# Kernel optimization log

Hardware: AMD Instinct MI355X
Metric: run time of the kernel (lower is better)

Reference implementation:

```python
import jax, jax.numpy as jnp
import numpy as np

INF = 1.0e12
V, EMB, H, H2 = 50000, 300, 512, 1024
EDGE, EEMB = 4, 32
B, TS, TQ = 16, 400, 33
MAX_OOV = 100
EXT = V + MAX_OOV
COV_HYPER = 1.0


def gru_cell(x, h, Wi, Wh, bi, bh):
    # torch GRU cell, gate order r,z,n
    gx = x @ Wi.T + bi
    gh = h @ Wh.T + bh
    hd = h.shape[-1]
    r = jax.nn.sigmoid(gx[:, :hd] + gh[:, :hd])
    z = jax.nn.sigmoid(gx[:, hd:2 * hd] + gh[:, hd:2 * hd])
    n = jnp.tanh(gx[:, 2 * hd:] + r * gh[:, 2 * hd:])
    return (1.0 - z) * n + z * h


def gru_scan(xs, h0, Wi, Wh, bi, bh, reverse=False):
    def step(h, x):
        hn = gru_cell(x, h, Wi, Wh, bi, bh)
        return hn, hn
    return jax.lax.scan(step, h0, xs, reverse=reverse)


def setup_inputs() -> dict:
    key = jax.random.key(0)
    ks = iter(jax.random.split(key, 64))
    def rp(*shape):
        return jax.random.normal(next(ks), shape, jnp.float32) * 0.05
    d = {}
    d['enc_emb'] = rp(V, EMB); d['ans_emb'] = rp(EDGE, EEMB); d['dec_emb'] = rp(V, EMB)
    in0 = EMB + EEMB
    d['eWi0'] = rp(2, 3 * H, in0); d['eWh0'] = rp(2, 3 * H, H); d['ebi0'] = rp(2, 3 * H); d['ebh0'] = rp(2, 3 * H)
    d['eWi1'] = rp(2, 3 * H, 2 * H); d['eWh1'] = rp(2, 3 * H, H); d['ebi1'] = rp(2, 3 * H); d['ebh1'] = rp(2, 3 * H)
    d['trans_W'] = rp(H2, H2); d['trans_b'] = rp(H2)
    d['upd_W'] = rp(H2, 2 * H2); d['gate_W'] = rp(H2, 2 * H2)
    din0 = EMB + H2
    d['dWi0'] = rp(3 * H2, din0); d['dWh0'] = rp(3 * H2, H2); d['dbi0'] = rp(3 * H2); d['dbh0'] = rp(3 * H2)
    d['dWi1'] = rp(3 * H2, H2); d['dWh1'] = rp(3 * H2, H2); d['dbi1'] = rp(3 * H2); d['dbh1'] = rp(3 * H2)
    d['dtrans_W'] = rp(H2, H2); d['dtrans_b'] = rp(H2)
    d['pW1'] = rp(H2, 2 * H2); d['pb1'] = rp(H2); d['pW2'] = rp(V, H2); d['pb2'] = rp(V)
    d['input_s'] = jax.random.randint(next(ks), (B, TS), 1, V)
    ext = jax.random.randint(next(ks), (B, TS), 0, EXT)
    d['ext_src_ids'] = ext.at[0, 0].set(EXT - 1)  # pin num_oov = MAX_OOV
    d['input_q'] = jax.random.randint(next(ks), (B, TQ), 1, V)
    d['input_a'] = jax.random.randint(next(ks), (B, TS), 0, EDGE)
    d['s_pos'] = jax.random.randint(next(ks), (B, TS), 0, TS)
    return d


def reference(enc_emb, ans_emb, dec_emb,
              eWi0, eWh0, ebi0, ebh0, eWi1, eWh1, ebi1, ebh1,
              trans_W, trans_b, upd_W, gate_W,
              dWi0, dWh0, dbi0, dbh0, dWi1, dWh1, dbi1, dbh1,
              dtrans_W, dtrans_b, pW1, pb1, pW2, pb2,
              input_s, ext_src_ids, input_q, input_a, s_pos):
    mask = jnp.sign(input_s)  # [B,TS] (all ones by construction)
    # ---------------- encoder ----------------
    emb = jnp.concatenate([enc_emb[input_s], ans_emb[input_a]], -1)  # [B,TS,EMB+EEMB]
    xs = emb.transpose(1, 0, 2)  # [TS,B,*]
    h0 = jnp.zeros((B, H), emb.dtype)
    h_list = []
    for (Wi, Wh, bi, bh) in ((eWi0, eWh0, ebi0, ebh0), (eWi1, eWh1, ebi1, ebh1)):
        hf, yf = gru_scan(xs, h0, Wi[0], Wh[0], bi[0], bh[0])
        hb, yb = gru_scan(xs, h0, Wi[1], Wh[1], bi[1], bh[1], reverse=True)
        xs = jnp.concatenate([yf, yb], -1)
        h_list.append(jnp.concatenate([hf, hb], -1))  # [B,H2]
    output = xs.transpose(1, 0, 2)  # [B,TS,H2]
    memories = output @ trans_W.T + trans_b
    # gated self-attention
    energies = jnp.einsum('btd,bsd->bts', output, memories)
    energies = jnp.where(mask[:, None, :] == 0, -INF, energies)
    scores = jax.nn.softmax(energies, -1)
    ctx = jnp.einsum('bts,bsd->btd', scores, output)
    inp = jnp.concatenate([output, ctx], -1)
    f_t = jnp.tanh(inp @ upd_W.T)
    g_t = jax.nn.sigmoid(inp @ gate_W.T)
    self_out = g_t * f_t + (1.0 - g_t) * output
    # answer-sentence attention (on memories, per original code)
    ans = jnp.where(input_a[..., None] == 0, 1.0, memories)
    e = memories * ans
    e = jnp.where(mask[..., None] == 0, -INF, e)
    e = jax.nn.softmax(e, axis=1)
    enc_out = self_out + e * memories
    # ---------------- decoder ----------------
    mem_d = enc_out @ dtrans_W.T + dtrans_b  # [B,TS,H2]
    emb_q = dec_emb[input_q[:, :-1]].transpose(1, 0, 2)  # [Tt,B,EMB]
    b_idx = jnp.arange(B)[:, None]

    def step(carry, emb_t):
        h0c, h1c, ctx_c, cov = carry
        rnn_in = jnp.concatenate([emb_t, ctx_c], -1)
        h0n = gru_cell(rnn_in, h0c, dWi0, dWh0, dbi0, dbh0)
        h1n = gru_cell(h0n, h1c, dWi1, dWh1, dbi1, dbh1)
        energy = jnp.einsum('bd,btd->bt', h1n, mem_d)
        sen_e = jnp.where(mask == 0, -INF, energy)
        cov_e = sen_e * (1.0 - cov)
        attn = jax.nn.softmax(cov_e, -1)
        new_ctx = jnp.einsum('bt,btd->bd', attn, mem_d)
        cov_loss = jnp.sum(jnp.minimum(attn, cov)) / B * COV_HYPER
        new_cov = cov + attn
        hid = jnp.tanh(jnp.concatenate([h1n, new_ctx], -1) @ pW1.T + pb1)
        logits = hid @ pW2.T + pb2
        ext = jnp.concatenate([logits, jnp.zeros((B, MAX_OOV), logits.dtype)], -1)
        out = jnp.full((B, EXT), -INF, logits.dtype).at[b_idx, ext_src_ids].max(cov_e)
        out = jnp.where(out == -INF, 0.0, out)
        lg = ext + out
        lg = jnp.where(lg == 0.0, -INF, lg)
        return (h0n, h1n, new_ctx, new_cov), (lg, cov_loss)

    init = (h_list[0], h_list[1], jnp.zeros((B, H2), emb.dtype), jnp.zeros((B, TS), emb.dtype))
    _, (lgs, covl) = jax.lax.scan(step, init, emb_q)
    return lgs.transpose(1, 0, 2), jnp.sum(covl) / lgs.shape[0]


if __name__ == '__main__':
    o = reference(**setup_inputs())
    print(o[0].shape, o[1])
```

## Files before the change

kernel.cpp:

```cpp
#include <hip/hip_runtime.h>
#include <stdint.h>

#define TSN 400
#define NB 16
#define HENC 512
#define HD2 1024
#define G3E 1536
#define G3D 3072
#define EMBD 300
#define AEMB 32
#define NV 50000
#define NEXT 50100
#define NVP 50176
#define NTT 32
#define NEG_INF (-1.0e12f)

typedef __attribute__((ext_vector_type(8))) short bf16x8;
typedef __attribute__((ext_vector_type(4))) float f32x4;

__device__ __forceinline__ ushort f2bf(float f) {
  unsigned u = __float_as_uint(f);
  unsigned r = (u + 0x7fffu + ((u >> 16) & 1u)) >> 16;
  return (ushort)r;
}
__device__ __forceinline__ float bf2f(ushort h) {
  return __uint_as_float((unsigned)h << 16);
}
__device__ __forceinline__ unsigned agat_ld(const unsigned* p) {
  return __hip_atomic_load(p, __ATOMIC_RELAXED, __HIP_MEMORY_SCOPE_AGENT);
}
__device__ __forceinline__ void agat_st(unsigned* p, unsigned v) {
  __hip_atomic_store(p, v, __ATOMIC_RELAXED, __HIP_MEMORY_SCOPE_AGENT);
}

__global__ __launch_bounds__(256) void k_embed_bf(
    const float* __restrict__ enc_emb, const float* __restrict__ ans_emb,
    const int* __restrict__ input_s, const int* __restrict__ input_a,
    ushort* __restrict__ X0)
{
  long i = (long)blockIdx.x*256 + threadIdx.x;
  if (i >= (long)TSN*NB*384) return;
  int c = (int)(i % 384);
  long r = i / 384;
  int b = (int)(r % NB);
  int t = (int)(r / NB);
  float v = 0.f;
  if (c < EMBD) v = enc_emb[(long)input_s[b*TSN + t]*EMBD + c];
  else if (c < 332) v = ans_emb[(long)input_a[b*TSN + t]*AEMB + (c - EMBD)];
  X0[i] = f2bf(v);
}

__global__ __launch_bounds__(256) void k_embq_bf(
    const float* __restrict__ dec_emb, const int* __restrict__ input_q,
    ushort* __restrict__ EQ)
{
  long i = (long)blockIdx.x*256 + threadIdx.x;
  if (i >= (long)NTT*NB*320) return;
  int c = (int)(i % 320);
  long r = i / 320;
  int b = (int)(r % NB);
  int s = (int)(r / NB);
  EQ[i] = (c < EMBD) ? f2bf(dec_emb[(long)input_q[b*33 + s]*EMBD + c]) : (ushort)0;
}

__global__ __launch_bounds__(256) void k_castw(
    const float* __restrict__ src, ushort* __restrict__ dst,
    int Nsrc, long total, int Ksrc, int Kdst, int ldsrc, int coloff)
{
  long i = (long)blockIdx.x*256 + threadIdx.x;
  if (i >= total) return;
  int k = (int)(i % Kdst);
  long n = i / Kdst;
  float v = (n < Nsrc && k < Ksrc) ? src[n*ldsrc + coloff + k] : 0.f;
  dst[i] = f2bf(v);
}

__global__ __launch_bounds__(256) void k_cast(
    const float* __restrict__ s, ushort* __restrict__ d, long n)
{
  long i = (long)blockIdx.x*256 + threadIdx.x;
  if (i >= n) return;
  d[i] = f2bf(s[i]);
}

__global__ __launch_bounds__(256) void k_catcopy(
    const unsigned* __restrict__ src, unsigned* __restrict__ dst)
{
  long i = (long)blockIdx.x*256 + threadIdx.x;
  if (i >= 6400l*512) return;
  long r = i >> 9;
  int c = (int)(i & 511);
  dst[(r << 10) + c] = src[i];
}

__global__ __launch_bounds__(256) void k_transpose_hh(
    const ushort* __restrict__ in, ushort* __restrict__ out)
{
  __shared__ ushort tb[32][33];
  int b = blockIdx.z;
  int r0 = blockIdx.x*32, c0 = blockIdx.y*32;
  int tx = threadIdx.x & 31, ty = threadIdx.x >> 5;
  #pragma unroll
  for (int i = 0; i < 32; i += 8) {
    int r = r0 + ty + i, c = c0 + tx;
    tb[ty+i][tx] = (r < TSN) ? in[((long)b*TSN + r)*1024 + c] : (ushort)0;
  }
  __syncthreads();
  #pragma unroll
  for (int i = 0; i < 32; i += 8) {
    int c = c0 + ty + i, r = r0 + tx;
    out[((long)b*1024 + c)*448 + r] = tb[tx][ty+i];
  }
}

__global__ __launch_bounds__(256) void k_mfma_nt(
    const ushort* __restrict__ Ab, const ushort* __restrict__ Wb,
    const float* __restrict__ bias, float* __restrict__ Cb, ushort* __restrict__ C2b,
    int M, int N, int K, int lda, int ldw, int ldc,
    long sA, long sW, long sC, long sBias, int accum, int act)
{
  __shared__ ushort As[64][72];
  __shared__ ushort Ws[64][72];
  const ushort* A = Ab + (long)blockIdx.z * sA;
  const ushort* W = Wb + (long)blockIdx.z * sW;
  float* C = Cb ? Cb + (long)blockIdx.z * sC : nullptr;
  const float* bi = bias ? bias + (long)blockIdx.z * sBias : nullptr;
  const int m0 = blockIdx.x*64, n0 = blockIdx.y*64;
  const int tid = threadIdx.x;
  const int wave = tid >> 6, lane = tid & 63;
  const int wm = wave >> 1, wn = wave & 1;
  const int lr = lane & 15, kg = lane >> 4;
  f32x4 acc[2][2] = {};
  for (int k0 = 0; k0 < K; k0 += 64) {
    __syncthreads();
    #pragma unroll
    for (int it = 0; it < 2; ++it) {
      int sidx = tid + it*256;
      int r = sidx >> 3, c = (sidx & 7)*8;
      bf16x8 av = {};
      bf16x8 wv = {};
      if (m0 + r < M) av = *(const bf16x8*)&A[(long)(m0+r)*lda + k0 + c];
      if (n0 + r < N) wv = *(const bf16x8*)&W[(long)(n0+r)*ldw + k0 + c];
      *(bf16x8*)&As[r][c] = av;
      *(bf16x8*)&Ws[r][c] = wv;
    }
    __syncthreads();
    #pragma unroll
    for (int kk = 0; kk < 2; ++kk) {
      bf16x8 af[2], bf[2];
      #pragma unroll
      for (int mt = 0; mt < 2; ++mt)
        af[mt] = *(const bf16x8*)&As[wm*32 + mt*16 + lr][kk*32 + kg*8];
      #pragma unroll
      for (int nt = 0; nt < 2; ++nt)
        bf[nt] = *(const bf16x8*)&Ws[wn*32 + nt*16 + lr][kk*32 + kg*8];
      #pragma unroll
      for (int mt = 0; mt < 2; ++mt)
        #pragma unroll
        for (int nt = 0; nt < 2; ++nt)
          acc[mt][nt] = __builtin_amdgcn_mfma_f32_16x16x32_bf16(af[mt], bf[nt], acc[mt][nt], 0, 0, 0);
    }
  }
  #pragma unroll
  for (int mt = 0; mt < 2; ++mt) {
    #pragma unroll
    for (int r = 0; r < 4; ++r) {
      int m = m0 + wm*32 + mt*16 + kg*4 + r;
      if (m >= M) continue;
      #pragma unroll
      for (int nt = 0; nt < 2; ++nt) {
        int n = n0 + wn*32 + nt*16 + lr;
        if (n >= N) continue;
        float v = acc[mt][nt][r];
        if (accum && C) v += C[(long)m*ldc + n];
        if (bi)    v += bi[n];
        if (act == 1) v = tanhf(v);
        else if (act == 2) v = 1.f/(1.f + expf(-v));
        if (C) C[(long)m*ldc + n] = v;
        if (C2b) C2b[(long)blockIdx.z*sC + (long)m*ldc + n] = f2bf(v);
      }
    }
  }
}

__global__ __launch_bounds__(256, 1) void k_scan_mfma(
    const ushort* __restrict__ GXf, const ushort* __restrict__ GXb,
    const ushort* __restrict__ Whb,
    const float* __restrict__ bh,
    ushort* __restrict__ Ybf, int bmajor,
    float* __restrict__ hfin,
    ushort* __restrict__ hpp,
    int* __restrict__ slots)
{
  const int bid = blockIdx.x;
  const int tid = threadIdx.x;
  const int wg = bid*4 + (tid >> 6);
  const int lane = tid & 63;
  const int lr = lane & 15, kg = lane >> 4;
  const int dir = wg >> 5, jt = wg & 31;
  const int j = jt*16 + lr;
  __shared__ ushort hsm[16][520];
  const ushort* Wp0 = Whb + ((long)(dir*G3E + j)        << 9) + kg*8;
  const ushort* Wp1 = Whb + ((long)(dir*G3E + 512 + j)  << 9) + kg*8;
  const ushort* Wp2 = Whb + ((long)(dir*G3E + 1024 + j) << 9) + kg*8;
  bf16x8 W0[16], W1[16], W2[16];
  #pragma unroll
  for (int i = 0; i < 16; ++i) {
    W0[i] = *(const bf16x8*)(Wp0 + i*32);
    W1[i] = *(const bf16x8*)(Wp1 + i*32);
    W2[i] = *(const bf16x8*)(Wp2 + i*32);
  }
  const float bh0 = bh[dir*G3E + j];
  const float bh1 = bh[dir*G3E + 512 + j];
  const float bh2 = bh[dir*G3E + 1024 + j];
  const ushort* GX = dir ? GXb : GXf;
  unsigned* hppu = (unsigned*)hpp;
  int* myslot = slots + dir*256 + (bid & 7)*32;
  int* dslots = slots + dir*256;
  float hreg[4] = {0.f, 0.f, 0.f, 0.f};
  float g0[4], g1[4], g2[4];
  {
    const int t0 = dir ? (TSN - 1) : 0;
    const ushort* gxp = GX + (long)t0*NB*G3E + j;
    #pragma unroll
    for (int r = 0; r < 4; ++r) {
      const ushort* g = gxp + (long)(kg*4 + r)*G3E;
      g0[r] = bf2f(g[0]); g1[r] = bf2f(g[512]); g2[r] = bf2f(g[1024]);
    }
  }
  for (int s = 0; s < TSN; ++s) {
    const int cur = s & 1;
    {
      const unsigned* hin = hppu + (cur*2 + dir)*4096;
      unsigned vdw[16];
      #pragma unroll
      for (int i = 0; i < 16; ++i) vdw[i] = agat_ld(hin + i*256 + tid);
      #pragma unroll
      for (int i = 0; i < 16; ++i) {
        int idx = i*256 + tid;
        int b = idx >> 8, jd = idx & 255;
        *(unsigned*)&hsm[b][jd*2] = vdw[i];
      }
    }
    __syncthreads();
    f32x4 a0 = {}, a1 = {}, a2 = {};
    #pragma unroll
    for (int i = 0; i < 16; ++i) {
      bf16x8 hf = *(const bf16x8*)&hsm[lr][kg*8 + i*32];
      a0 = __builtin_amdgcn_mfma_f32_16x16x32_bf16(hf, W0[i], a0, 0, 0, 0);
      a1 = __builtin_amdgcn_mfma_f32_16x16x32_bf16(hf, W1[i], a1, 0, 0, 0);
      a2 = __builtin_amdgcn_mfma_f32_16x16x32_bf16(hf, W2[i], a2, 0, 0, 0);
    }
    const int t = dir ? (TSN - 1 - s) : s;
    const int obase = ((cur^1)*2 + dir)*16*512;
    float hsave[4];
    #pragma unroll
    for (int r = 0; r < 4; ++r) {
      int b = kg*4 + r;
      float rr = 1.f/(1.f + expf(-(g0[r] + a0[r] + bh0)));
      float zz = 1.f/(1.f + expf(-(g1[r] + a1[r] + bh1)));
      float nn = tanhf(g2[r] + rr*(a2[r] + bh2));
      float hn = (1.f - zz)*nn + zz*hreg[r];
      hreg[r] = hn;
      hsave[r] = hn;
      unsigned hv = f2bf(hn);
      unsigned pv = (unsigned)__shfl_xor((int)hv, 1);
      if ((lr & 1) == 0)
        agat_st(hppu + ((obase + b*512 + j) >> 1), hv | (pv << 16));
    }
    if (s + 1 < TSN) {
      asm volatile("s_waitcnt vmcnt(0)" ::: "memory");
      __syncthreads();
      if (tid == 0)
        agat_st((unsigned*)myslot, (unsigned)(s + 1));
      {
        const int tn = dir ? (TSN - 2 - s) : (s + 1);
        const ushort* gxp = GX + (long)tn*NB*G3E + j;
        #pragma unroll
        for (int r = 0; r < 4; ++r) {
          const ushort* g = gxp + (long)(kg*4 + r)*G3E;
          g0[r] = bf2f(g[0]); g1[r] = bf2f(g[512]); g2[r] = bf2f(g[1024]);
        }
      }
      #pragma unroll
      for (int r = 0; r < 4; ++r) {
        int b = kg*4 + r;
        long yi = bmajor ? ((long)b*TSN + t)*1024 + dir*512 + j
                         : ((long)t*NB + b)*1024 + dir*512 + j;
        Ybf[yi] = f2bf(hsave[r]);
      }
      if (tid < 8) {
        while ((int)agat_ld((const unsigned*)(dslots + tid*32)) < s + 1)
          __builtin_amdgcn_s_sleep(1);
      }
      __syncthreads();
    } else {
      #pragma unroll
      for (int r = 0; r < 4; ++r) {
        int b = kg*4 + r;
        long yi = bmajor ? ((long)b*TSN + t)*1024 + dir*512 + j
                         : ((long)t*NB + b)*1024 + dir*512 + j;
        Ybf[yi] = f2bf(hsave[r]);
        hfin[b*1024 + dir*512 + j] = hsave[r];
      }
    }
  }
}

__global__ __launch_bounds__(256) void k_softmax_bf(
    const float* __restrict__ E, ushort* __restrict__ S)
{
  long row = blockIdx.x;
  const float* x = E + row*TSN;
  ushort* o = S + row*448;
  int tid = threadIdx.x;
  float v0 = (tid < TSN) ? x[tid] : -INFINITY;
  float v1 = (tid + 256 < TSN) ? x[tid + 256] : -INFINITY;
  __shared__ float red[256];
  red[tid] = fmaxf(v0, v1); __syncthreads();
  for (int oo = 128; oo; oo >>= 1) { if (tid < oo) red[tid] = fmaxf(red[tid], red[tid+oo]); __syncthreads(); }
  float m = red[0]; __syncthreads();
  float e0 = (tid < TSN) ? expf(v0 - m) : 0.f;
  float e1 = (tid + 256 < TSN) ? expf(v1 - m) : 0.f;
  red[tid] = e0 + e1; __syncthreads();
  for (int oo = 128; oo; oo >>= 1) { if (tid < oo) red[tid] += red[tid+oo]; __syncthreads(); }
  float inv = 1.f/red[0];
  if (tid < 192) o[tid + 256] = (tid + 256 < TSN) ? f2bf(e1*inv) : (ushort)0;
  o[tid] = f2bf(e0*inv);
}

__global__ __launch_bounds__(256) void k_ansatt2(
    const ushort* __restrict__ memsb, const ushort* __restrict__ ftgt,
    const ushort* __restrict__ outpb,
    const int* __restrict__ input_a, ushort* __restrict__ encb)
{
  int b = blockIdx.x >> 2;
  int d = (blockIdx.x & 3)*256 + threadIdx.x;
  __shared__ int ia[TSN];
  for (int i = threadIdx.x; i < TSN; i += 256) ia[i] = input_a[b*TSN + i];
  __syncthreads();
  float m = -INFINITY;
  #pragma unroll 4
  for (int t = 0; t < TSN; ++t) {
    float v = bf2f(memsb[((long)b*TSN + t)*1024 + d]);
    float e = ia[t] ? v*v : v;
    m = fmaxf(m, e);
  }
  float ssum = 0.f;
  #pragma unroll 4
  for (int t = 0; t < TSN; ++t) {
    float v = bf2f(memsb[((long)b*TSN + t)*1024 + d]);
    float e = ia[t] ? v*v : v;
    ssum += expf(e - m);
  }
  float inv = 1.f/ssum;
  #pragma unroll 4
  for (int t = 0; t < TSN; ++t) {
    long idx = ((long)b*TSN + t)*1024 + d;
    long idx2 = ((long)b*TSN + t)*2048 + d;
    float v = bf2f(memsb[idx]);
    float e = ia[t] ? v*v : v;
    float fraw = bf2f(ftgt[idx2]);
    float graw = bf2f(ftgt[idx2 + 1024]);
    float gg = 1.f/(1.f + expf(-graw));
    float selfo = gg*tanhf(fraw) + (1.f - gg)*bf2f(outpb[idx]);
    encb[idx] = f2bf(selfo + expf(e - m)*inv*v);
  }
}

__global__ __launch_bounds__(128) void k_gru_dec(
    const ushort* __restrict__ A1, const ushort* __restrict__ W1,
    const ushort* __restrict__ A2, const ushort* __restrict__ W2,
    const float* __restrict__ gxadd, const float* __restrict__ bi,
    const float* __restrict__ bh,
    const float* __restrict__ hprev, float* __restrict__ hout,
    ushort* __restrict__ houtb, ushort* __restrict__ catb)
{
  const int wv = threadIdx.x >> 6;
  const int lane = threadIdx.x & 63;
  const int lr = lane & 15, kg = lane >> 4;
  const int j = blockIdx.x*16 + lr;
  const int kb = wv*512;
  __shared__ float psum[6][16][16];
  const ushort* w1p0 = W1 + ((long)(j)        << 10) + kb + kg*8;
  const ushort* w1p1 = W1 + ((long)(1024 + j) << 10) + kb + kg*8;
  const ushort* w1p2 = W1 + ((long)(2048 + j) << 10) + kb + kg*8;
  const ushort* w2p0 = W2 + ((long)(j)        << 10) + kb + kg*8;
  const ushort* w2p1 = W2 + ((long)(1024 + j) << 10) + kb + kg*8;
  const ushort* w2p2 = W2 + ((long)(2048 + j) << 10) + kb + kg*8;
  const ushort* a1p = A1 + lr*1024 + kb + kg*8;
  const ushort* a2p = A2 + lr*1024 + kb + kg*8;
  f32x4 x0 = {}, x1 = {}, x2 = {}, h0 = {}, h1 = {}, h2 = {};
  #pragma unroll 4
  for (int k0 = 0; k0 < 512; k0 += 32) {
    bf16x8 a1v = *(const bf16x8*)(a1p + k0);
    bf16x8 a2v = *(const bf16x8*)(a2p + k0);
    x0 = __builtin_amdgcn_mfma_f32_16x16x32_bf16(a1v, *(const bf16x8*)(w1p0 + k0), x0, 0, 0, 0);
    x1 = __builtin_amdgcn_mfma_f32_16x16x32_bf16(a1v, *(const bf16x8*)(w1p1 + k0), x1, 0, 0, 0);
    x2 = __builtin_amdgcn_mfma_f32_16x16x32_bf16(a1v, *(const bf16x8*)(w1p2 + k0), x2, 0, 0, 0);
    h0 = __builtin_amdgcn_mfma_f32_16x16x32_bf16(a2v, *(const bf16x8*)(w2p0 + k0), h0, 0, 0, 0);
    h1 = __builtin_amdgcn_mfma_f32_16x16x32_bf16(a2v, *(const bf16x8*)(w2p1 + k0), h1, 0, 0, 0);
    h2 = __builtin_amdgcn_mfma_f32_16x16x32_bf16(a2v, *(const bf16x8*)(w2p2 + k0), h2, 0, 0, 0);
  }
  if (wv == 1) {
    #pragma unroll
    for (int r = 0; r < 4; ++r) {
      int b = kg*4 + r;
      psum[0][b][lr] = x0[r]; psum[1][b][lr] = x1[r]; psum[2][b][lr] = x2[r];
      psum[3][b][lr] = h0[r]; psum[4][b][lr] = h1[r]; psum[5][b][lr] = h2[r];
    }
  }
  __syncthreads();
  if (wv == 0) {
    float bi0 = bi ? bi[j] : 0.f, bi1 = bi ? bi[1024 + j] : 0.f, bi2 = bi ? bi[2048 + j] : 0.f;
    float bh0 = bh[j], bh1 = bh[1024 + j], bh2 = bh[2048 + j];
    #pragma unroll
    for (int r = 0; r < 4; ++r) {
      int b = kg*4 + r;
      float gxa0 = gxadd ? gxadd[(long)b*G3D + j]        : 0.f;
      float gxa1 = gxadd ? gxadd[(long)b*G3D + 1024 + j] : 0.f;
      float gxa2 = gxadd ? gxadd[(long)b*G3D + 2048 + j] : 0.f;
      float gx0 = x0[r] + psum[0][b][lr] + gxa0 + bi0;
      float gx1 = x1[r] + psum[1][b][lr] + gxa1 + bi1;
      float gx2 = x2[r] + psum[2][b][lr] + gxa2 + bi2;
      float gh0 = h0[r] + psum[3][b][lr] + bh0;
      float gh1 = h1[r] + psum[4][b][lr] + bh1;
      float gh2 = h2[r] + psum[5][b][lr] + bh2;
      float rr = 1.f/(1.f + expf(-(gx0 + gh0)));
      float zz = 1.f/(1.f + expf(-(gx1 + gh1)));
      float nn = tanhf(gx2 + rr*gh2);
      float hp = hprev[b*1024 + j];
      float hn = (1.f - zz)*nn + zz*hp;
      hout[b*1024 + j] = hn;
      houtb[b*1024 + j] = f2bf(hn);
      if (catb) catb[(long)b*2048 + j] = f2bf(hn);
    }
  }
}

__global__ __launch_bounds__(256) void k_dec_attn3(
    const ushort* __restrict__ h1b, const ushort* __restrict__ memdb,
    float* __restrict__ cov, float* __restrict__ coveS, float* __restrict__ covacc,
    float* __restrict__ scb,
    ushort* __restrict__ ctxn, ushort* __restrict__ catb,
    int* __restrict__ slots, int epoch)
{
  const int bid = blockIdx.x, tid = threadIdx.x;
  const int b = bid >> 2, q = bid & 3;
  const int wv = tid >> 6, lane = tid & 63;
  __shared__ float at[TSN];
  __shared__ float red[256];
  __shared__ float psD[4][64][4];
  float hr[16];
  {
    bf16x8 hv0 = *(const bf16x8*)&h1b[b*1024 + lane*16];
    bf16x8 hv1 = *(const bf16x8*)&h1b[b*1024 + lane*16 + 8];
    #pragma unroll
    for (int e = 0; e < 8; ++e) { hr[e] = bf2f((ushort)hv0[e]); hr[8+e] = bf2f((ushort)hv1[e]); }
// ... 89 lines not shown
  const int lr = lane & 15, kg = lane >> 4;
  const int n = blockIdx.x*16 + lr;
  const int kb = wv*1024;
  __shared__ float ps[16][16];
  f32x4 acc = {};
  const ushort* ap = catb + lr*2048 + kb + kg*8;
  const ushort* wp = W + ((long)n << 11) + kb + kg*8;
  #pragma unroll 8
  for (int k0 = 0; k0 < 1024; k0 += 32)
    acc = __builtin_amdgcn_mfma_f32_16x16x32_bf16(*(const bf16x8*)(ap + k0), *(const bf16x8*)(wp + k0), acc, 0, 0, 0);
  if (wv == 1) {
    #pragma unroll
    for (int r = 0; r < 4; ++r) ps[kg*4 + r][lr] = acc[r];
  }
  __syncthreads();
  if (wv == 0) {
    float bv = pb1[n];
    #pragma unroll
    for (int r = 0; r < 4; ++r) {
      int b = kg*4 + r;
      hidb[b*1024 + n] = f2bf(tanhf(acc[r] + ps[b][lr] + bv));
    }
  }
}

__global__ __launch_bounds__(256) void k_logits_all(
    const ushort* __restrict__ hidAll,
    const ushort* __restrict__ pW2b,
    const float* __restrict__ pb2,
    float* __restrict__ outp)
{
  const int wave = threadIdx.x >> 6, lane = threadIdx.x & 63;
  const int lr = lane & 15, kg = lane >> 4;
  const int n0 = blockIdx.x*256 + wave*64;
  const int m0 = blockIdx.y*128;
  f32x4 acc[8][4] = {};
  for (int k0 = 0; k0 < 1024; k0 += 32) {
    bf16x8 bfr[4];
    #pragma unroll
    for (int nt = 0; nt < 4; ++nt)
      bfr[nt] = *(const bf16x8*)&pW2b[(long)(n0 + nt*16 + lr)*1024 + k0 + kg*8];
    #pragma unroll
    for (int mt = 0; mt < 8; ++mt) {
      bf16x8 af = *(const bf16x8*)&hidAll[(long)(m0 + mt*16 + lr)*1024 + k0 + kg*8];
      #pragma unroll
      for (int nt = 0; nt < 4; ++nt)
        acc[mt][nt] = __builtin_amdgcn_mfma_f32_16x16x32_bf16(af, bfr[nt], acc[mt][nt], 0, 0, 0);
    }
  }
  #pragma unroll
  for (int nt = 0; nt < 4; ++nt) {
    int v = n0 + nt*16 + lr;
    if (v >= NEXT) continue;
    float pb = (v < NV) ? pb2[v] : 0.f;
    #pragma unroll
    for (int mt = 0; mt < 8; ++mt) {
      #pragma unroll
      for (int r = 0; r < 4; ++r) {
        int m = m0 + mt*16 + kg*4 + r;
        int s = m >> 4, b = m & 15;
        float e = (v < NV) ? (acc[mt][nt][r] + pb) : 0.f;
        if (e == 0.f) e = NEG_INF;
        outp[((long)b*NTT + s)*NEXT + v] = e;
      }
    }
  }
}

__device__ __forceinline__ float dec_f(unsigned e) {
  return (e & 0x80000000u) ? __uint_as_float(e ^ 0x80000000u) : __uint_as_float(~e);
}
__global__ __launch_bounds__(512) void k_compose_all(
    const int* __restrict__ ids, const float* __restrict__ coveAll,
    unsigned* __restrict__ ubuf, float* __restrict__ outp)
{
  int b = blockIdx.x, tid = threadIdx.x;
  int v = 0;
  if (tid < TSN) v = ids[b*TSN + tid];
  unsigned* up = ubuf + (long)b*NEXT;
  for (int s = 0; s < NTT; ++s) {
    if (tid < TSN) {
      float ce = coveAll[((long)s*NB + b)*TSN + tid];
      unsigned bb = __float_as_uint(ce);
      unsigned enc = (bb & 0x80000000u) ? ~bb : (bb | 0x80000000u);
      atomicMax(&up[v], enc);
    }
    __syncthreads();
    if (tid < TSN) {
      unsigned u = __hip_atomic_load(&up[v], __ATOMIC_RELAXED, __HIP_MEMORY_SCOPE_AGENT);
      float o = dec_f(u);
      long oi = ((long)b*NTT + s)*NEXT + v;
      float e = outp[oi];
      if (e == NEG_INF) e = 0.f;
      float lg = e + o;
      if (lg == 0.f) lg = NEG_INF;
      outp[oi] = lg;
    }
    __syncthreads();
    if (tid < TSN)
      __hip_atomic_store(&up[v], 0u, __ATOMIC_RELAXED, __HIP_MEMORY_SCOPE_AGENT);
    __syncthreads();
  }
}

__global__ void k_covout(const float* __restrict__ covacc, float* __restrict__ outp)
{
  outp[(long)NB*NTT*NEXT] = covacc[0] * (1.0f/(NB*NTT));
}

extern "C" void kernel_launch(void* const* d_in, const int* in_sizes, int n_in,
                              void* d_out, int out_size, void* d_ws, size_t ws_size,
                              hipStream_t stream) {
  (void)in_sizes; (void)n_in; (void)out_size; (void)ws_size;
  const float* enc_emb = (const float*)d_in[0];
  const float* ans_emb = (const float*)d_in[1];
  const float* dec_emb = (const float*)d_in[2];
  const float* eWi0 = (const float*)d_in[3];
  const float* eWh0 = (const float*)d_in[4];
  const float* ebi0 = (const float*)d_in[5];
  const float* ebh0 = (const float*)d_in[6];
  const float* eWi1 = (const float*)d_in[7];
  const float* eWh1 = (const float*)d_in[8];
  const float* ebi1 = (const float*)d_in[9];
  const float* ebh1 = (const float*)d_in[10];
  const float* trans_W = (const float*)d_in[11];
  const float* trans_b = (const float*)d_in[12];
  const float* upd_W = (const float*)d_in[13];
  const float* gate_W = (const float*)d_in[14];
  const float* dWi0 = (const float*)d_in[15];
  const float* dWh0 = (const float*)d_in[16];
  const float* dbi0 = (const float*)d_in[17];
  const float* dbh0 = (const float*)d_in[18];
  const float* dWi1 = (const float*)d_in[19];
  const float* dWh1 = (const float*)d_in[20];
  const float* dbi1 = (const float*)d_in[21];
  const float* dbh1 = (const float*)d_in[22];
  const float* dtrans_W = (const float*)d_in[23];
  const float* dtrans_b = (const float*)d_in[24];
  const float* pW1 = (const float*)d_in[25];
  const float* pb1 = (const float*)d_in[26];
  const float* pW2 = (const float*)d_in[27];
  const float* pb2 = (const float*)d_in[28];
  const int* input_s = (const int*)d_in[29];
  const int* ext_ids = (const int*)d_in[30];
  const int* input_q = (const int*)d_in[31];
  const int* input_a = (const int*)d_in[32];
  float* out = (float*)d_out;

  float* ws = (float*)d_ws;
  size_t off = 0;
  auto alloc = [&](size_t n) { float* p = ws + off; off += (n + 15) & ~(size_t)15; return p; };
  auto alloch = [&](size_t nh) { return (ushort*)alloc((nh + 1) / 2); };

  ushort* hpp  = alloch(2ull*2*NB*HENC);
  int*   bar   = (int*)alloc(4096);
  float* covacc= alloc(4);
  float* cov   = alloc(NB*TSN);
  float* scb   = alloc(NB*TSN);
  unsigned* ubuf = (unsigned*)alloc((size_t)NB*NEXT);
  float* hfin0 = alloc(NB*HD2);
  float* hfin1 = alloc(NB*HD2);
  float* dh0   = alloc(2ull*NB*HD2);
  float* dh1   = alloc(2ull*NB*HD2);
  ushort* h0b  = alloch(2ull*NB*HD2);
  ushort* h1b  = alloch(2ull*NB*HD2);
  ushort* ctxbf= alloch(2ull*NB*HD2);
  ushort* catbf= alloch((size_t)NB*2048);
  ushort* hidAll = alloch((size_t)NTT*NB*HD2);
  float* coveAll = alloc((size_t)NTT*NB*TSN);

  ushort* eWi0c   = alloch(2ull*G3E*384);
  ushort* eWi1c   = alloch(2ull*G3E*1024);
  ushort* Whb0    = alloch(2ull*G3E*HENC);
  ushort* Whb1    = alloch(2ull*G3E*HENC);
  ushort* transWb = alloch(1024ull*1024);
  ushort* fgWb    = alloch(2048ull*2048);
  ushort* dtransWb= alloch(1024ull*1024);
  ushort* dWi0e   = alloch(3072ull*320);
  ushort* dWi0c   = alloch(3072ull*1024);
  ushort* dWh0b   = alloch(3072ull*1024);
  ushort* dWi1b   = alloch(3072ull*1024);
  ushort* dWh1b   = alloch(3072ull*1024);
  ushort* pW1b    = alloch(1024ull*2048);

  size_t regionStart = off;
  float*  GXr  = alloc(2ull*6400*G3E);
  ushort* GXbf = (ushort*)GXr;
  ushort* X0c  = alloch(6400ull*384);
  ushort* Y0bf = alloch(6400ull*1024);
  alloc(6400ull*HD2);
  ushort* ftgt_bf = (ushort*)(ws + regionStart);
  ushort* pW2b    = (ushort*)(ws + regionStart);
  ushort* outpTb  = (ushort*)(ws + regionStart + 26000000);

  ushort* outpbf = alloch(6400ull*HD2);
  ushort* memsbf = alloch(6400ull*HD2);
  ushort* catE   = alloch(6400ull*2048);
  float*  energ  = alloc((size_t)NB*TSN*TSN);
  ushort* scoresb= alloch((size_t)NB*TSN*448);
  ushort* memd_bf= alloch(6400ull*HD2);
  ushort* encbf  = alloch(6400ull*HD2);
  ushort* embqb  = alloch(512ull*320);
  float*  embGX  = alloc(512ull*G3D);

  k_embed_bf<<<9600, 256, 0, stream>>>(enc_emb, ans_emb, input_s, input_a, X0c);
  k_castw<<<4608, 256, 0, stream>>>(eWi0, eWi0c, 3072, 3072ull*384, 332, 384, 332, 0);
  k_castw<<<12288, 256, 0, stream>>>(eWi1, eWi1c, 3072, 3072ull*1024, 1024, 1024, 1024, 0);
  k_castw<<<6144, 256, 0, stream>>>(eWh0, Whb0, 3072, 3072ull*512, 512, 512, 512, 0);
  k_castw<<<6144, 256, 0, stream>>>(eWh1, Whb1, 3072, 3072ull*512, 512, 512, 512, 0);
  k_castw<<<4096, 256, 0, stream>>>(trans_W, transWb, 1024, 1024ull*1024, 1024, 1024, 1024, 0);
  k_castw<<<8192, 256, 0, stream>>>(upd_W,  fgWb,              1024, 1024ull*2048, 2048, 2048, 2048, 0);
  k_castw<<<8192, 256, 0, stream>>>(gate_W, fgWb + 1024ull*2048, 1024, 1024ull*2048, 2048, 2048, 2048, 0);
  k_castw<<<4096, 256, 0, stream>>>(dtrans_W, dtransWb, 1024, 1024ull*1024, 1024, 1024, 1024, 0);
  k_castw<<<3840, 256, 0, stream>>>(dWi0, dWi0e, 3072, 3072ull*320, 300, 320, 1324, 0);
  k_castw<<<12288, 256, 0, stream>>>(dWi0, dWi0c, 3072, 3072ull*1024, 1024, 1024, 1324, 300);
  k_castw<<<12288, 256, 0, stream>>>(dWh0, dWh0b, 3072, 3072ull*1024, 1024, 1024, 1024, 0);
  k_castw<<<12288, 256, 0, stream>>>(dWi1, dWi1b, 3072, 3072ull*1024, 1024, 1024, 1024, 0);
  k_castw<<<12288, 256, 0, stream>>>(dWh1, dWh1b, 3072, 3072ull*1024, 1024, 1024, 1024, 0);
  k_castw<<<8192, 256, 0, stream>>>(pW1, pW1b, 1024, 1024ull*2048, 2048, 2048, 2048, 0);

  hipMemsetAsync(bar, 0, 16384, stream);

  k_mfma_nt<<<dim3(100,24,2), 256, 0, stream>>>(X0c, eWi0c, ebi0, nullptr, GXbf,
      6400, G3E, 384, 384, 384, G3E, 0, (long)G3E*384, 6400ull*G3E, G3E, 0, 0);
  hipMemsetAsync(hpp, 0, 2ull*2*NB*HENC*2, stream);
  k_scan_mfma<<<16, 256, 0, stream>>>(GXbf, GXbf + 6400ull*G3E, Whb0, ebh0,
      Y0bf, 0, hfin0, hpp, bar);
  k_mfma_nt<<<dim3(100,24,2), 256, 0, stream>>>(Y0bf, eWi1c, ebi1, nullptr, GXbf,
      6400, G3E, 1024, 1024, 1024, G3E, 0, (long)G3E*1024, 6400ull*G3E, G3E, 0, 0);
  hipMemsetAsync(hpp, 0, 2ull*2*NB*HENC*2, stream);
  k_scan_mfma<<<16, 256, 0, stream>>>(GXbf, GXbf + 6400ull*G3E, Whb1, ebh1,
      outpbf, 1, hfin1, hpp, bar + 512);

  k_mfma_nt<<<dim3(100,16,1), 256, 0, stream>>>(outpbf, transWb, trans_b, nullptr, memsbf,
      6400, HD2, 1024, 1024, 1024, HD2, 0, 0, 0, 0, 0, 0);
  k_mfma_nt<<<dim3(7,7,16), 256, 0, stream>>>(outpbf, memsbf, nullptr, energ, nullptr,
      TSN, TSN, 1024, 1024, 1024, TSN, (long)TSN*1024, (long)TSN*1024, (long)TSN*TSN, 0, 0, 0);
  k_softmax_bf<<<NB*TSN, 256, 0, stream>>>(energ, scoresb);
  k_transpose_hh<<<dim3(14,32,16), 256, 0, stream>>>(outpbf, outpTb);
  k_mfma_nt<<<dim3(7,16,16), 256, 0, stream>>>(scoresb, outpTb, nullptr, nullptr, catE + 1024,
      TSN, HD2, 448, 448, 448, 2048, (long)TSN*448, (long)HD2*448, (long)TSN*2048, 0, 0, 0);
  k_catcopy<<<12800, 256, 0, stream>>>((const unsigned*)outpbf, (unsigned*)catE);
  k_mfma_nt<<<dim3(100,32,1), 256, 0, stream>>>(catE, fgWb, nullptr, nullptr, ftgt_bf,
      6400, 2048, 2048, 2048, 2048, 2048, 0, 0, 0, 0, 0, 0);
  k_ansatt2<<<64, 256, 0, stream>>>(memsbf, ftgt_bf, outpbf, input_a, encbf);
  k_castw<<<200704, 256, 0, stream>>>(pW2, pW2b, NV, (long)NVP*1024, 1024, 1024, 1024, 0);
  k_mfma_nt<<<dim3(100,16,1), 256, 0, stream>>>(encbf, dtransWb, dtrans_b, nullptr, memd_bf,
      6400, HD2, 1024, 1024, 1024, HD2, 0, 0, 0, 0, 0, 0);

  k_embq_bf<<<640, 256, 0, stream>>>(dec_emb, input_q, embqb);
  k_mfma_nt<<<dim3(8,48,1), 256, 0, stream>>>(embqb, dWi0e, dbi0, embGX, nullptr,
      NTT*NB, G3D, 320, 320, 320, G3D, 0, 0, 0, 0, 0, 0);

  hipMemsetAsync(cov, 0, (size_t)NB*TSN*4, stream);
  hipMemsetAsync(covacc, 0, 4, stream);
  hipMemsetAsync(ubuf, 0, (size_t)NB*NEXT*4, stream);
  hipMemsetAsync(ctxbf, 0, (size_t)NB*HD2*2, stream);
  hipMemcpyAsync(dh0, hfin0, (size_t)NB*HD2*4, hipMemcpyDeviceToDevice, stream);
  hipMemcpyAsync(dh1, hfin1, (size_t)NB*HD2*4, hipMemcpyDeviceToDevice, stream);
  k_cast<<<64, 256, 0, stream>>>(hfin0, h0b, 16384);
  k_cast<<<64, 256, 0, stream>>>(hfin1, h1b, 16384);

  for (int s = 0; s < NTT; ++s) {
    int cur = s & 1, nxt = cur ^ 1;
    float* h0c = dh0 + (size_t)cur*NB*HD2;  float* h0n = dh0 + (size_t)nxt*NB*HD2;
    float* h1c = dh1 + (size_t)cur*NB*HD2;  float* h1n = dh1 + (size_t)nxt*NB*HD2;
    ushort* h0bc = h0b + (size_t)cur*NB*HD2; ushort* h0bn = h0b + (size_t)nxt*NB*HD2;
    ushort* h1bc = h1b + (size_t)cur*NB*HD2; ushort* h1bn = h1b + (size_t)nxt*NB*HD2;
    ushort* ctxc = ctxbf + (size_t)cur*NB*HD2; ushort* ctxn = ctxbf + (size_t)nxt*NB*HD2;

    k_gru_dec<<<64, 128, 0, stream>>>(ctxc, dWi0c, h0bc, dWh0b,
        embGX + (size_t)s*NB*G3D, nullptr, dbh0, h0c, h0n, h0bn, nullptr);
    k_gru_dec<<<64, 128, 0, stream>>>(h0bn, dWi1b, h1bc, dWh1b,
        nullptr, dbi1, dbh1, h1c, h1n, h1bn, catbf);
    k_dec_attn3<<<64, 256, 0, stream>>>(h1bn, memd_bf,
        cov, coveAll + (size_t)s*NB*TSN, covacc, scb, ctxn, catbf,
        bar + 1024, s + 1);
    k_hid<<<64, 128, 0, stream>>>(catbf, pW1b, pb1, hidAll + (size_t)s*NB*HD2);
  }
  k_logits_all<<<dim3(196, 4), 256, 0, stream>>>(hidAll, pW2b, pb2, out);
  k_compose_all<<<NB, 512, 0, stream>>>(ext_ids, coveAll, ubuf, out);
  k_covout<<<1, 1, 0, stream>>>(covacc, out);
}
```

Measured before the change: 6.001 ms.

## Replace cross-block MFMA GRU scan with per-batch fp16 dot2 scan kernels

```diff
diff --git a/kernel.cpp b/kernel.cpp
--- a/kernel.cpp
+++ b/kernel.cpp
@@ -17,6 +17,7 @@
 
 typedef __attribute__((ext_vector_type(8))) short bf16x8;
 typedef __attribute__((ext_vector_type(4))) float f32x4;
+typedef _Float16 f16x2 __attribute__((ext_vector_type(2)));
 
 __device__ __forceinline__ ushort f2bf(float f) {
   unsigned u = __float_as_uint(f);
@@ -31,6 +32,9 @@
 }
 __device__ __forceinline__ void agat_st(unsigned* p, unsigned v) {
   __hip_atomic_store(p, v, __ATOMIC_RELAXED, __HIP_MEMORY_SCOPE_AGENT);
+}
+__device__ __forceinline__ f16x2 u2h(unsigned u) {
+  union { unsigned x; f16x2 h; } c; c.x = u; return c.h;
 }
 
 __global__ __launch_bounds__(256) void k_embed_bf(
@@ -73,6 +77,26 @@
   long n = i / Kdst;
   float v = (n < Nsrc && k < Ksrc) ? src[n*ldsrc + coloff + k] : 0.f;
   dst[i] = f2bf(v);
+}
+
+__global__ __launch_bounds__(256) void k_castw_scan(
+    const float* __restrict__ src, unsigned* __restrict__ dst)
+{
+  long i = (long)blockIdx.x*256 + threadIdx.x;
+  if (i >= 786432l) return;
+  int dir = (int)(i / 393216);
+  int rem = (int)(i % 393216);
+  int p = rem / 1536;
+  int q = rem % 1536;
+  int jp = q / 6;
+  int g2 = q % 6;
+  int g = g2 >> 1, je = g2 & 1;
+  int row = g*512 + 2*jp + je;
+  const float* s = src + (long)dir*1536*512 + (long)row*512 + 2*p;
+  union { _Float16 h[2]; unsigned u; } c;
+  c.h[0] = (_Float16)s[0];
+  c.h[1] = (_Float16)s[1];
+  dst[i] = c.u;
 }
 
 __global__ __launch_bounds__(256) void k_cast(
@@ -183,127 +207,73 @@
   }
 }
 
-__global__ __launch_bounds__(256, 1) void k_scan_mfma(
+__global__ __launch_bounds__(256, 1) void k_scan_seq(
     const ushort* __restrict__ GXf, const ushort* __restrict__ GXb,
-    const ushort* __restrict__ Whb,
+    const unsigned* __restrict__ Wv,
     const float* __restrict__ bh,
     ushort* __restrict__ Ybf, int bmajor,
-    float* __restrict__ hfin,
-    ushort* __restrict__ hpp,
-    int* __restrict__ slots)
+    float* __restrict__ hfin)
 {
   const int bid = blockIdx.x;
+  const int b = bid >> 1, dir = bid & 1;
   const int tid = threadIdx.x;
-  const int wg = bid*4 + (tid >> 6);
-  const int lane = tid & 63;
-  const int lr = lane & 15, kg = lane >> 4;
-  const int dir = wg >> 5, jt = wg & 31;
-  const int j = jt*16 + lr;
-  __shared__ ushort hsm[16][520];
-  const ushort* Wp0 = Whb + ((long)(dir*G3E + j)        << 9) + kg*8;
-  const ushort* Wp1 = Whb + ((long)(dir*G3E + 512 + j)  << 9) + kg*8;
-  const ushort* Wp2 = Whb + ((long)(dir*G3E + 1024 + j) << 9) + kg*8;
-  bf16x8 W0[16], W1[16], W2[16];
-  #pragma unroll
-  for (int i = 0; i < 16; ++i) {
-    W0[i] = *(const bf16x8*)(Wp0 + i*32);
-    W1[i] = *(const bf16x8*)(Wp1 + i*32);
-    W2[i] = *(const bf16x8*)(Wp2 + i*32);
-  }
-  const float bh0 = bh[dir*G3E + j];
-  const float bh1 = bh[dir*G3E + 512 + j];
-  const float bh2 = bh[dir*G3E + 1024 + j];
+  const int j0 = 2*tid;
+  __shared__ unsigned hbuf[2][256];
   const ushort* GX = dir ? GXb : GXf;
-  unsigned* hppu = (unsigned*)hpp;
-  int* myslot = slots + dir*256 + (bid & 7)*32;
-  int* dslots = slots + dir*256;
-  float hreg[4] = {0.f, 0.f, 0.f, 0.f};
-  float g0[4], g1[4], g2[4];
-  {
-    const int t0 = dir ? (TSN - 1) : 0;
-    const ushort* gxp = GX + (long)t0*NB*G3E + j;
-    #pragma unroll
-    for (int r = 0; r < 4; ++r) {
-      const ushort* g = gxp + (long)(kg*4 + r)*G3E;
-      g0[r] = bf2f(g[0]); g1[r] = bf2f(g[512]); g2[r] = bf2f(g[1024]);
-    }
-  }
+  const unsigned* wbase = Wv + (long)dir*393216 + tid*6;
+  const float br0 = bh[dir*G3E + j0],        br1 = bh[dir*G3E + j0 + 1];
+  const float bz0 = bh[dir*G3E + 512 + j0],  bz1 = bh[dir*G3E + 512 + j0 + 1];
+  const float bn0 = bh[dir*G3E + 1024 + j0], bn1 = bh[dir*G3E + 1024 + j0 + 1];
+  float h0 = 0.f, h1 = 0.f;
+  hbuf[0][tid] = 0u;
+  __syncthreads();
   for (int s = 0; s < TSN; ++s) {
     const int cur = s & 1;
+    const int t = dir ? (TSN - 1 - s) : s;
+    const unsigned* gxp = (const unsigned*)(GX + ((long)t*NB + b)*G3E);
+    unsigned gr = gxp[tid];
+    unsigned gz = gxp[256 + tid];
+    unsigned gn = gxp[512 + tid];
+    float a0 = 0.f, a1 = 0.f, a2 = 0.f, a3 = 0.f, a4 = 0.f, a5 = 0.f;
+    const unsigned* wp = wbase;
+    const unsigned* hl = hbuf[cur];
+    #pragma unroll 4
+    for (int p = 0; p < 256; ++p) {
+      f16x2 hh = u2h(hl[p]);
+      a0 = __builtin_amdgcn_fdot2(hh, u2h(wp[0]), a0, false);
+      a1 = __builtin_amdgcn_fdot2(hh, u2h(wp[1]), a1, false);
+      a2 = __builtin_amdgcn_fdot2(hh, u2h(wp[2]), a2, false);
+      a3 = __builtin_amdgcn_fdot2(hh, u2h(wp[3]), a3, false);
+      a4 = __builtin_amdgcn_fdot2(hh, u2h(wp[4]), a4, false);
+      a5 = __builtin_amdgcn_fdot2(hh, u2h(wp[5]), a5, false);
+      wp += 1536;
+    }
+    float gr0 = bf2f((ushort)(gr & 0xffffu)), gr1 = bf2f((ushort)(gr >> 16));
+    float gz0 = bf2f((ushort)(gz & 0xffffu)), gz1 = bf2f((ushort)(gz >> 16));
+    float gn0 = bf2f((ushort)(gn & 0xffffu)), gn1 = bf2f((ushort)(gn >> 16));
+    float r0 = 1.f/(1.f + expf(-(gr0 + a0 + br0)));
+    float r1 = 1.f/(1.f + expf(-(gr1 + a1 + br1)));
+    float z0 = 1.f/(1.f + expf(-(gz0 + a2 + bz0)));
+    float z1 = 1.f/(1.f + expf(-(gz1 + a3 + bz1)));
+    float n0 = tanhf(gn0 + r0*(a4 + bn0));
+    float n1 = tanhf(gn1 + r1*(a5 + bn1));
+    float hn0 = (1.f - z0)*n0 + z0*h0;
+    float hn1 = (1.f - z1)*n1 + z1*h1;
+    h0 = hn0; h1 = hn1;
     {
-      const unsigned* hin = hppu + (cur*2 + dir)*4096;
-      unsigned vdw[16];
-      #pragma unroll
-      for (int i = 0; i < 16; ++i) vdw[i] = agat_ld(hin + i*256 + tid);
-      #pragma unroll
-      for (int i = 0; i < 16; ++i) {
-        int idx = i*256 + tid;
-        int b = idx >> 8, jd = idx & 255;
-        *(unsigned*)&hsm[b][jd*2] = vdw[i];
-      }
+      union { _Float16 h[2]; unsigned u; } c;
+      c.h[0] = (_Float16)hn0; c.h[1] = (_Float16)hn1;
+      hbuf[cur^1][tid] = c.u;
+    }
+    unsigned yv = (unsigned)f2bf(hn0) | ((unsigned)f2bf(hn1) << 16);
+    long yi = bmajor ? ((long)b*TSN + t)*1024 + dir*512 + j0
+                     : ((long)t*NB + b)*1024 + dir*512 + j0;
+    *(unsigned*)&Ybf[yi] = yv;
+    if (s == TSN - 1) {
+      hfin[b*1024 + dir*512 + j0]     = hn0;
+      hfin[b*1024 + dir*512 + j0 + 1] = hn1;
     }
     __syncthreads();
-    f32x4 a0 = {}, a1 = {}, a2 = {};
-    #pragma unroll
-    for (int i = 0; i < 16; ++i) {
-      bf16x8 hf = *(const bf16x8*)&hsm[lr][kg*8 + i*32];
-      a0 = __builtin_amdgcn_mfma_f32_16x16x32_bf16(hf, W0[i], a0, 0, 0, 0);
-      a1 = __builtin_amdgcn_mfma_f32_16x16x32_bf16(hf, W1[i], a1, 0, 0, 0);
-      a2 = __builtin_amdgcn_mfma_f32_16x16x32_bf16(hf, W2[i], a2, 0, 0, 0);
-    }
-    const int t = dir ? (TSN - 1 - s) : s;
-    const int obase = ((cur^1)*2 + dir)*16*512;
-    float hsave[4];
-    #pragma unroll
-    for (int r = 0; r < 4; ++r) {
-      int b = kg*4 + r;
-      float rr = 1.f/(1.f + expf(-(g0[r] + a0[r] + bh0)));
-      float zz = 1.f/(1.f + expf(-(g1[r] + a1[r] + bh1)));
-      float nn = tanhf(g2[r] + rr*(a2[r] + bh2));
-      float hn = (1.f - zz)*nn + zz*hreg[r];
-      hreg[r] = hn;
-      hsave[r] = hn;
-      unsigned hv = f2bf(hn);
-      unsigned pv = (unsigned)__shfl_xor((int)hv, 1);
-      if ((lr & 1) == 0)
-        agat_st(hppu + ((obase + b*512 + j) >> 1), hv | (pv << 16));
-    }
-    if (s + 1 < TSN) {
-      asm volatile("s_waitcnt vmcnt(0)" ::: "memory");
-      __syncthreads();
-      if (tid == 0)
-        agat_st((unsigned*)myslot, (unsigned)(s + 1));
-      {
-        const int tn = dir ? (TSN - 2 - s) : (s + 1);
-        const ushort* gxp = GX + (long)tn*NB*G3E + j;
-        #pragma unroll
-        for (int r = 0; r < 4; ++r) {
-          const ushort* g = gxp + (long)(kg*4 + r)*G3E;
-          g0[r] = bf2f(g[0]); g1[r] = bf2f(g[512]); g2[r] = bf2f(g[1024]);
-        }
-      }
-      #pragma unroll
-      for (int r = 0; r < 4; ++r) {
-        int b = kg*4 + r;
-        long yi = bmajor ? ((long)b*TSN + t)*1024 + dir*512 + j
-                         : ((long)t*NB + b)*1024 + dir*512 + j;
-        Ybf[yi] = f2bf(hsave[r]);
-      }
-      if (tid < 8) {
-        while ((int)agat_ld((const unsigned*)(dslots + tid*32)) < s + 1)
-          __builtin_amdgcn_s_sleep(1);
-      }
-      __syncthreads();
-    } else {
-      #pragma unroll
-      for (int r = 0; r < 4; ++r) {
-        int b = kg*4 + r;
-        long yi = bmajor ? ((long)b*TSN + t)*1024 + dir*512 + j
-                         : ((long)t*NB + b)*1024 + dir*512 + j;
-        Ybf[yi] = f2bf(hsave[r]);
-        hfin[b*1024 + dir*512 + j] = hsave[r];
-      }
-    }
   }
 }
 
@@ -699,7 +669,6 @@
   auto alloc = [&](size_t n) { float* p = ws + off; off += (n + 15) & ~(size_t)15; return p; };
   auto alloch = [&](size_t nh) { return (ushort*)alloc((nh + 1) / 2); };
 
-  ushort* hpp  = alloch(2ull*2*NB*HENC);
   int*   bar   = (int*)alloc(4096);
   float* covacc= alloc(4);
   float* cov   = alloc(NB*TSN);
@@ -718,8 +687,8 @@
 
   ushort* eWi0c   = alloch(2ull*G3E*384);
   ushort* eWi1c   = alloch(2ull*G3E*1024);
-  ushort* Whb0    = alloch(2ull*G3E*HENC);
-  ushort* Whb1    = alloch(2ull*G3E*HENC);
+  unsigned* Wv0   = (unsigned*)alloc(786432);
+  unsigned* Wv1   = (unsigned*)alloc(786432);
   ushort* transWb = alloch(1024ull*1024);
   ushort* fgWb    = alloch(2048ull*2048);
   ushort* dtransWb= alloch(1024ull*1024);
@@ -753,8 +722,8 @@
   k_embed_bf<<<9600, 256, 0, stream>>>(enc_emb, ans_emb, input_s, input_a, X0c);
   k_castw<<<4608, 256, 0, stream>>>(eWi0, eWi0c, 3072, 3072ull*384, 332, 384, 332, 0);
   k_castw<<<12288, 256, 0, stream>>>(eWi1, eWi1c, 3072, 3072ull*1024, 1024, 1024, 1024, 0);
-  k_castw<<<6144, 256, 0, stream>>>(eWh0, Whb0, 3072, 3072ull*512, 512, 512, 512, 0);
-  k_castw<<<6144, 256, 0, stream>>>(eWh1, Whb1, 3072, 3072ull*512, 512, 512, 512, 0);
+  k_castw_scan<<<3072, 256, 0, stream>>>(eWh0, Wv0);
+  k_castw_scan<<<3072, 256, 0, stream>>>(eWh1, Wv1);
   k_castw<<<4096, 256, 0, stream>>>(trans_W, transWb, 1024, 1024ull*1024, 1024, 1024, 1024, 0);
   k_castw<<<8192, 256, 0, stream>>>(upd_W,  fgWb,              1024, 1024ull*2048, 2048, 2048, 2048, 0);
   k_castw<<<8192, 256, 0, stream>>>(gate_W, fgWb + 1024ull*2048, 1024, 1024ull*2048, 2048, 2048, 2048, 0);
@@ -770,14 +739,12 @@
 
   k_mfma_nt<<<dim3(100,24,2), 256, 0, stream>>>(X0c, eWi0c, ebi0, nullptr, GXbf,
       6400, G3E, 384, 384, 384, G3E, 0, (long)G3E*384, 6400ull*G3E, G3E, 0, 0);
-  hipMemsetAsync(hpp, 0, 2ull*2*NB*HENC*2, stream);
-  k_scan_mfma<<<16, 256, 0, stream>>>(GXbf, GXbf + 6400ull*G3E, Whb0, ebh0,
-      Y0bf, 0, hfin0, hpp, bar);
+  k_scan_seq<<<32, 256, 0, stream>>>(GXbf, GXbf + 6400ull*G3E, Wv0, ebh0,
+      Y0bf, 0, hfin0);
   k_mfma_nt<<<dim3(100,24,2), 256, 0, stream>>>(Y0bf, eWi1c, ebi1, nullptr, GXbf,
       6400, G3E, 1024, 1024, 1024, G3E, 0, (long)G3E*1024, 6400ull*G3E, G3E, 0, 0);
-  hipMemsetAsync(hpp, 0, 2ull*2*NB*HENC*2, stream);
-  k_scan_mfma<<<16, 256, 0, stream>>>(GXbf, GXbf + 6400ull*G3E, Whb1, ebh1,
-      outpbf, 1, hfin1, hpp, bar + 512);
+  k_scan_seq<<<32, 256, 0, stream>>>(GXbf, GXbf + 6400ull*G3E, Wv1, ebh1,
+      outpbf, 1, hfin1);
 
   k_mfma_nt<<<dim3(100,16,1), 256, 0, stream>>>(outpbf, transWb, trans_b, nullptr, memsbf,
       6400, HD2, 1024, 1024, 1024, HD2, 0, 0, 0, 0, 0, 0);
```

After: 16.28 ms. 2.71x slower.

## Replace scan slot barrier with step-tagged 64-bit hidden-state exchange

Applied to the files above, without the earlier changes.

```diff
diff --git a/kernel.cpp b/kernel.cpp
--- a/kernel.cpp
+++ b/kernel.cpp
@@ -30,6 +30,12 @@
   return __hip_atomic_load(p, __ATOMIC_RELAXED, __HIP_MEMORY_SCOPE_AGENT);
 }
 __device__ __forceinline__ void agat_st(unsigned* p, unsigned v) {
+  __hip_atomic_store(p, v, __ATOMIC_RELAXED, __HIP_MEMORY_SCOPE_AGENT);
+}
+__device__ __forceinline__ unsigned long long agat_ld64(const unsigned long long* p) {
+  return __hip_atomic_load(p, __ATOMIC_RELAXED, __HIP_MEMORY_SCOPE_AGENT);
+}
+__device__ __forceinline__ void agat_st64(unsigned long long* p, unsigned long long v) {
   __hip_atomic_store(p, v, __ATOMIC_RELAXED, __HIP_MEMORY_SCOPE_AGENT);
 }
 
@@ -189,8 +195,7 @@
     const float* __restrict__ bh,
     ushort* __restrict__ Ybf, int bmajor,
     float* __restrict__ hfin,
-    ushort* __restrict__ hpp,
-    int* __restrict__ slots)
+    unsigned long long* __restrict__ hex)
 {
   const int bid = blockIdx.x;
   const int tid = threadIdx.x;
@@ -214,32 +219,40 @@
   const float bh1 = bh[dir*G3E + 512 + j];
   const float bh2 = bh[dir*G3E + 1024 + j];
   const ushort* GX = dir ? GXb : GXf;
-  unsigned* hppu = (unsigned*)hpp;
-  int* myslot = slots + dir*256 + (bid & 7)*32;
-  int* dslots = slots + dir*256;
   float hreg[4] = {0.f, 0.f, 0.f, 0.f};
-  float g0[4], g1[4], g2[4];
-  {
-    const int t0 = dir ? (TSN - 1) : 0;
-    const ushort* gxp = GX + (long)t0*NB*G3E + j;
-    #pragma unroll
-    for (int r = 0; r < 4; ++r) {
-      const ushort* g = gxp + (long)(kg*4 + r)*G3E;
-      g0[r] = bf2f(g[0]); g1[r] = bf2f(g[512]); g2[r] = bf2f(g[1024]);
-    }
-  }
   for (int s = 0; s < TSN; ++s) {
     const int cur = s & 1;
+    const int t = dir ? (TSN - 1 - s) : s;
+    float g0[4], g1[4], g2[4];
     {
-      const unsigned* hin = hppu + (cur*2 + dir)*4096;
-      unsigned vdw[16];
+      const ushort* gxp = GX + ((long)t*NB)*G3E + j;
       #pragma unroll
-      for (int i = 0; i < 16; ++i) vdw[i] = agat_ld(hin + i*256 + tid);
+      for (int r = 0; r < 4; ++r) {
+        const ushort* g = gxp + (long)(kg*4 + r)*G3E;
+        g0[r] = bf2f(g[0]); g1[r] = bf2f(g[512]); g2[r] = bf2f(g[1024]);
+      }
+    }
+    {
+      const unsigned long long* hx = hex + ((size_t)((cur<<1) + dir) << 12);
+      unsigned hdat[16];
+      unsigned pending = 0xffffu;
+      while (pending) {
+        #pragma unroll
+        for (int i = 0; i < 16; ++i) {
+          if (pending & (1u << i)) {
+            unsigned long long v = agat_ld64(hx + i*256 + tid);
+            if ((unsigned)(v >> 32) == (unsigned)s) {
+              hdat[i] = (unsigned)v;
+              pending &= ~(1u << i);
+            }
+          }
+        }
+        if (pending) __builtin_amdgcn_s_sleep(1);
+      }
       #pragma unroll
       for (int i = 0; i < 16; ++i) {
         int idx = i*256 + tid;
-        int b = idx >> 8, jd = idx & 255;
-        *(unsigned*)&hsm[b][jd*2] = vdw[i];
+        *(unsigned*)&hsm[idx >> 8][(idx & 255)*2] = hdat[i];
       }
     }
     __syncthreads();
@@ -251,9 +264,7 @@
       a1 = __builtin_amdgcn_mfma_f32_16x16x32_bf16(hf, W1[i], a1, 0, 0, 0);
       a2 = __builtin_amdgcn_mfma_f32_16x16x32_bf16(hf, W2[i], a2, 0, 0, 0);
     }
-    const int t = dir ? (TSN - 1 - s) : s;
-    const int obase = ((cur^1)*2 + dir)*16*512;
-    float hsave[4];
+    unsigned long long* ho = hex + ((size_t)(((cur^1)<<1) + dir) << 12);
     #pragma unroll
     for (int r = 0; r < 4; ++r) {
       int b = kg*4 + r;
@@ -262,48 +273,19 @@
       float nn = tanhf(g2[r] + rr*(a2[r] + bh2));
       float hn = (1.f - zz)*nn + zz*hreg[r];
       hreg[r] = hn;
-      hsave[r] = hn;
       unsigned hv = f2bf(hn);
       unsigned pv = (unsigned)__shfl_xor((int)hv, 1);
-      if ((lr & 1) == 0)
-        agat_st(hppu + ((obase + b*512 + j) >> 1), hv | (pv << 16));
-    }
-    if (s + 1 < TSN) {
-      asm volatile("s_waitcnt vmcnt(0)" ::: "memory");
-      __syncthreads();
-      if (tid == 0)
-        agat_st((unsigned*)myslot, (unsigned)(s + 1));
-      {
-        const int tn = dir ? (TSN - 2 - s) : (s + 1);
-        const ushort* gxp = GX + (long)tn*NB*G3E + j;
-        #pragma unroll
-        for (int r = 0; r < 4; ++r) {
-          const ushort* g = gxp + (long)(kg*4 + r)*G3E;
-          g0[r] = bf2f(g[0]); g1[r] = bf2f(g[512]); g2[r] = bf2f(g[1024]);
-        }
+      if ((lr & 1) == 0) {
+        unsigned long long pack = ((unsigned long long)(unsigned)(s + 1) << 32)
+                                | (unsigned long long)(hv | (pv << 16));
+        agat_st64(ho + (b*256 + (j >> 1)), pack);
       }
-      #pragma unroll
-      for (int r = 0; r < 4; ++r) {
-        int b = kg*4 + r;
-        long yi = bmajor ? ((long)b*TSN + t)*1024 + dir*512 + j
-                         : ((long)t*NB + b)*1024 + dir*512 + j;
-        Ybf[yi] = f2bf(hsave[r]);
-      }
-      if (tid < 8) {
-        while ((int)agat_ld((const unsigned*)(dslots + tid*32)) < s + 1)
-          __builtin_amdgcn_s_sleep(1);
-      }
-      __syncthreads();
-    } else {
-      #pragma unroll
-      for (int r = 0; r < 4; ++r) {
-        int b = kg*4 + r;
-        long yi = bmajor ? ((long)b*TSN + t)*1024 + dir*512 + j
-                         : ((long)t*NB + b)*1024 + dir*512 + j;
-        Ybf[yi] = f2bf(hsave[r]);
-        hfin[b*1024 + dir*512 + j] = hsave[r];
-      }
-    }
+      long yi = bmajor ? ((long)b*TSN + t)*1024 + dir*512 + j
+                       : ((long)t*NB + b)*1024 + dir*512 + j;
+      Ybf[yi] = f2bf(hn);
+      if (s == TSN - 1) hfin[b*1024 + dir*512 + j] = hn;
+    }
+    __syncthreads();
   }
 }
 
@@ -699,7 +681,7 @@
   auto alloc = [&](size_t n) { float* p = ws + off; off += (n + 15) & ~(size_t)15; return p; };
   auto alloch = [&](size_t nh) { return (ushort*)alloc((nh + 1) / 2); };
 
-  ushort* hpp  = alloch(2ull*2*NB*HENC);
+  unsigned long long* hex = (unsigned long long*)alloc(32768);
   int*   bar   = (int*)alloc(4096);
   float* covacc= alloc(4);
   float* cov   = alloc(NB*TSN);
@@ -770,14 +752,14 @@
 
   k_mfma_nt<<<dim3(100,24,2), 256, 0, stream>>>(X0c, eWi0c, ebi0, nullptr, GXbf,
       6400, G3E, 384, 384, 384, G3E, 0, (long)G3E*384, 6400ull*G3E, G3E, 0, 0);
-  hipMemsetAsync(hpp, 0, 2ull*2*NB*HENC*2, stream);
+  hipMemsetAsync(hex, 0, 131072, stream);
   k_scan_mfma<<<16, 256, 0, stream>>>(GXbf, GXbf + 6400ull*G3E, Whb0, ebh0,
-      Y0bf, 0, hfin0, hpp, bar);
+      Y0bf, 0, hfin0, hex);
   k_mfma_nt<<<dim3(100,24,2), 256, 0, stream>>>(Y0bf, eWi1c, ebi1, nullptr, GXbf,
       6400, G3E, 1024, 1024, 1024, G3E, 0, (long)G3E*1024, 6400ull*G3E, G3E, 0, 0);
-  hipMemsetAsync(hpp, 0, 2ull*2*NB*HENC*2, stream);
+  hipMemsetAsync(hex, 0, 131072, stream);
   k_scan_mfma<<<16, 256, 0, stream>>>(GXbf, GXbf + 6400ull*G3E, Whb1, ebh1,
-      outpbf, 1, hfin1, hpp, bar + 512);
+      outpbf, 1, hfin1, hex);
 
   k_mfma_nt<<<dim3(100,16,1), 256, 0, stream>>>(outpbf, transWb, trans_b, nullptr, memsbf,
       6400, HD2, 1024, 1024, 1024, HD2, 0, 0, 0, 0, 0, 0);
```

Result: slower. 8.689 ms (+44.8%).
